# Kernel optimization log

Measured on AMD Instinct MI355X. Metric: run time of the kernel, lower is better.

The kernel has to match this reference:

```python
import jax, jax.numpy as jnp
import numpy as np

NF = 10      # num RBF / Chebyshev features
GAMMA = 1.0
EMB = 10
H = 64
NHEADS = 2


def _rbf(d):
    centers = jnp.arange(1, NF + 1, dtype=d.dtype)
    return jnp.exp(-GAMMA * (centers - d[..., None]) ** 2)


def _cheb(a):
    feats = [jnp.ones_like(a), a]
    for _ in range(2, NF):
        feats.append(2 * a * feats[-1] - feats[-2])
    return jnp.stack(feats, -1)


def _gru_layer(xs, wih, whh, bih, bhh):
    # xs: [L, B, D] -> [L, B, H]; PyTorch gate order r, z, n
    B = xs.shape[1]
    def step(h, xt):
        gi = xt @ wih.T + bih
        gh = h @ whh.T + bhh
        ir, iz, inn = jnp.split(gi, 3, -1)
        hr, hz, hn = jnp.split(gh, 3, -1)
        r = jax.nn.sigmoid(ir + hr)
        z = jax.nn.sigmoid(iz + hz)
        n = jnp.tanh(inn + r * hn)
        hnew = (1 - z) * n + z * h
        return hnew, hnew
    h0 = jnp.zeros((B, H), xs.dtype)
    _, ys = jax.lax.scan(step, h0, xs)
    return ys


def _mha(x, in_w, in_b, out_w, out_b):
    B, L, E = x.shape
    hd = E // NHEADS
    qkv = x @ in_w.T + in_b
    q, k, v = jnp.split(qkv, 3, -1)
    sp = lambda t: t.reshape(B, L, NHEADS, hd).transpose(0, 2, 1, 3)
    q, k, v = sp(q), sp(k), sp(v)
    scale = 1.0 / float(np.sqrt(hd))
    att = jax.nn.softmax(jnp.einsum('bhqd,bhkd->bhqk', q, k) * scale, -1)
    o = jnp.einsum('bhqk,bhkd->bhqd', att, v).transpose(0, 2, 1, 3).reshape(B, L, E)
    return o @ out_w.T + out_b


def _ln(x, s, b):
    m = x.mean(-1, keepdims=True)
    v = ((x - m) ** 2).mean(-1, keepdims=True)
    return (x - m) / jnp.sqrt(v + 1e-5) * s + b


def setup_inputs() -> dict:
    key = jax.random.key(0)
    ks = jax.random.split(key, 48)
    N, L = 384, 256
    # bond rows: [atom_idx1, atom_idx2, bond_dist]; angle rows: [d1, d2, angle]
    idx1 = jax.random.randint(ks[0], (N, L), 1, 119).astype(jnp.float32)
    idx2 = jax.random.randint(ks[1], (N, L), 1, 119).astype(jnp.float32)
    dist = jax.random.uniform(ks[2], (N, L), minval=0.5, maxval=5.0)
    d1 = jax.random.uniform(ks[3], (N, L), minval=0.5, maxval=5.0)
    d2 = jax.random.uniform(ks[4], (N, L), minval=0.5, maxval=5.0)
    ang = jax.random.uniform(ks[5], (N, L), minval=-1.0, maxval=1.0)
    bond_x = jnp.stack([idx1, idx2, dist], 1)
    angle_x = jnp.stack([d1, d2, ang], 1)
    is_angle = (jnp.arange(N) % 3 == 2)
    x = jnp.where(is_angle[:, None, None], angle_x, bond_x)

    def nrm(k, shp, s=0.1):
        return jax.random.normal(k, shp) * s

    D_IN = 2 * EMB + NF  # 30
    inp = {
        'x': x,
        'emb': nrm(ks[6], (119, EMB), 1.0),
        'wih0': nrm(ks[7], (3 * H, D_IN)),
        'whh0': nrm(ks[8], (3 * H, H)),
        'bih0': nrm(ks[9], (3 * H,)),
        'bhh0': nrm(ks[10], (3 * H,)),
        'wih12': nrm(ks[11], (2, 3 * H, H)),
        'whh12': nrm(ks[12], (2, 3 * H, H)),
        'bih12': nrm(ks[13], (2, 3 * H)),
        'bhh12': nrm(ks[14], (2, 3 * H)),
        'in_w1': nrm(ks[15], (3 * H, H)),
        'in_b1': nrm(ks[16], (3 * H,)),
        'out_w1': nrm(ks[17], (H, H)),
        'out_b1': nrm(ks[18], (H,)),
        'in_w2': nrm(ks[19], (3 * H, H)),
        'in_b2': nrm(ks[20], (3 * H,)),
        'out_w2': nrm(ks[21], (H, H)),
        'out_b2': nrm(ks[22], (H,)),
        'ff_w1': nrm(ks[23], (1024, H)),
        'ff_b1': nrm(ks[24], (1024,)),
        'ff_w2': nrm(ks[25], (H, 1024)),
        'ff_b2': nrm(ks[26], (H,)),
        'ln1_s': jnp.ones((H,)), 'ln1_b': jnp.zeros((H,)),
        'ln2_s': jnp.ones((H,)), 'ln2_b': jnp.zeros((H,)),
        'ln3_s': jnp.ones((H,)), 'ln3_b': jnp.zeros((H,)),
        'ln4_s': jnp.ones((H,)), 'ln4_b': jnp.zeros((H,)),
        'fw1': nrm(ks[27], (256, H)), 'fb1': nrm(ks[28], (256,)),
        'fw2': nrm(ks[29], (64, 256)), 'fb2': nrm(ks[30], (64,)),
        'fw3': nrm(ks[31], (32, 64)), 'fb3': nrm(ks[32], (32,)),
        'fw4': nrm(ks[33], (1, 32)), 'fb4': nrm(ks[34], (1,)),
    }
    return inp


def reference(x, emb, wih0, whh0, bih0, bhh0, wih12, whh12, bih12, bhh12,
              in_w1, in_b1, out_w1, out_b1, in_w2, in_b2, out_w2, out_b2,
              ff_w1, ff_b1, ff_w2, ff_b2,
              ln1_s, ln1_b, ln2_s, ln2_b, ln3_s, ln3_b, ln4_s, ln4_b,
              fw1, fb1, fw2, fb2, fw3, fb3, fw4, fb4):
    # Vectorized featurization (replaces the per-triplet Python loop):
    # rows with i%3 in {0,1} are bond rows, i%3==2 are angle rows.
    i1 = jnp.clip(x[:, 0].astype(jnp.int32), 0, 118)
    i2 = jnp.clip(x[:, 1].astype(jnp.int32), 0, 118)
    bond_feat = jnp.concatenate([emb[i1], emb[i2], _rbf(x[:, 2])], -1)
    angle_feat = jnp.concatenate([_rbf(x[:, 0]), _rbf(x[:, 1]), _cheb(x[:, 2])], -1)
    is_angle = (jnp.arange(x.shape[0]) % 3 == 2)
    feat = jnp.where(is_angle[:, None, None], angle_feat, bond_feat)  # [N, L, 30]

    hs = feat.transpose(1, 0, 2)  # [L, N, 30]
    hs = _gru_layer(hs, wih0, whh0, bih0, bhh0)
    for l in range(2):
        hs = _gru_layer(hs, wih12[l], whh12[l], bih12[l], bhh12[l])
    g = hs.transpose(1, 0, 2)  # [N, L, H]

    def ffn(t):
        return jax.nn.relu(jax.nn.relu(t @ ff_w1.T + ff_b1) @ ff_w2.T + ff_b2)

    a = _mha(g, in_w1, in_b1, out_w1, out_b1)
    h = _ln(g + a, ln1_s, ln1_b)
    h = _ln(h + ffn(h), ln2_s, ln2_b)
    a = _mha(h, in_w2, in_b2, out_w2, out_b2)
    h = _ln(a + a, ln3_s, ln3_b)  # faithful to original: attn_out + attn_out
    h = _ln(h + ffn(h), ln4_s, ln4_b)
    o = h[:, -1, :]
    o = jax.nn.silu(o @ fw1.T + fb1)
    o = jax.nn.silu(o @ fw2.T + fb2)
    o = jax.nn.silu(o @ fw3.T + fb3)
    o = o @ fw4.T + fb4
    return o.squeeze(-1)
```

## Files before the change

### kernel.cpp

```cpp
#include <hip/hip_runtime.h>

static constexpr int NB   = 384;
static constexpr int SEQL = 256;
static constexpr int NROWS = NB * SEQL;

typedef short bf16x8 __attribute__((ext_vector_type(8)));
typedef float f32x4  __attribute__((ext_vector_type(4)));

union B8u {
    bf16x8 v;
    ushort us[8];
    uint4  q;
};

__device__ inline ushort f2bf(float f) {
    uint u = __float_as_uint(f);
    uint r = u + 0x7FFFu + ((u >> 16) & 1u);
    return (ushort)(r >> 16);
}

__device__ inline void split8(float4 a, float4 b, B8u& hi, B8u& lo) {
    float f[8] = {a.x, a.y, a.z, a.w, b.x, b.y, b.z, b.w};
    #pragma unroll
    for (int i = 0; i < 8; ++i) {
        ushort h = f2bf(f[i]);
        hi.us[i] = h;
        float fh = __uint_as_float(((uint)h) << 16);
        lo.us[i] = f2bf(f[i] - fh);
    }
}

__global__ __launch_bounds__(256) void split_kernel(
    const float* __restrict__ src, ushort* __restrict__ hi,
    ushort* __restrict__ lo, int n)
{
    int i = blockIdx.x * 256 + threadIdx.x;
    if (i < n) {
        float f = src[i];
        ushort h = f2bf(f);
        hi[i] = h;
        float fh = __uint_as_float(((uint)h) << 16);
        lo[i] = f2bf(f - fh);
    }
}

__global__ __launch_bounds__(192) void featproj_kernel(
    const float* __restrict__ x, const float* __restrict__ emb,
    const float* __restrict__ wih0, const float* __restrict__ bih0,
    float* __restrict__ X)
{
    __shared__ float F[32][33];
    const int tid = threadIdx.x;
    const int m0  = blockIdx.x * 32;

    if (tid < 96) {
        const int r   = tid & 31;
        const int grp = tid >> 5;
        const int m   = m0 + r;
        const int b   = m % NB;
        const int l   = m / NB;
        const float* xb = x + (size_t)b * (3 * SEQL);
        const float x0 = xb[l], x1 = xb[SEQL + l], x2 = xb[2 * SEQL + l];
        const bool is_angle = (b % 3) == 2;
        float o[10];
        if (is_angle) {
            if (grp < 2) {
                const float a = (grp == 0) ? x0 : x1;
                #pragma unroll
                for (int c = 0; c < 10; ++c) { float d = (float)(c + 1) - a; o[c] = __expf(-d * d); }
            } else {
                float t0 = 1.f, t1 = x2;
                o[0] = 1.f; o[1] = x2;
                #pragma unroll
                for (int c = 2; c < 10; ++c) { float t = 2.f * x2 * t1 - t0; o[c] = t; t0 = t1; t1 = t; }
            }
        } else {
            if (grp < 2) {
                const float xv = (grp == 0) ? x0 : x1;
                int idx = (int)xv; idx = idx < 0 ? 0 : (idx > 118 ? 118 : idx);
                #pragma unroll
                for (int c = 0; c < 10; ++c) o[c] = emb[idx * 10 + c];
            } else {
                #pragma unroll
                for (int c = 0; c < 10; ++c) { float d = (float)(c + 1) - x2; o[c] = __expf(-d * d); }
            }
        }
        #pragma unroll
        for (int c = 0; c < 10; ++c) F[r][grp * 10 + c] = o[c];
    }
    __syncthreads();

    float w[30];
    #pragma unroll
    for (int k = 0; k < 30; ++k) w[k] = wih0[tid * 30 + k];
    const float bj = bih0[tid];
    for (int r = 0; r < 32; ++r) {
        float acc = bj;
        #pragma unroll
        for (int k = 0; k < 30; ++k) acc += F[r][k] * w[k];
        X[(size_t)(m0 + r) * 192 + tid] = acc;
    }
}

__global__ __launch_bounds__(192) void gru_kernel(
    const float* __restrict__ X, const float* __restrict__ whh,
    const float* __restrict__ bhh, float* __restrict__ Y, int out_batch_major)
{
    const int b = blockIdx.x;
    const int j = threadIdx.x;
    __shared__ float h[64];
    __shared__ float gis[192], ghs[192];

    float w[64];
    #pragma unroll
    for (int k = 0; k < 64; ++k) w[k] = whh[j * 64 + k];
    const float bj = bhh[j];
    if (j < 64) h[j] = 0.f;
    __syncthreads();

    for (int t = 0; t < SEQL; ++t) {
        const float gi = X[((size_t)t * NB + b) * 192 + j];
        float gh = bj;
        #pragma unroll
        for (int k = 0; k < 64; ++k) gh += h[k] * w[k];
        gis[j] = gi; ghs[j] = gh;
        __syncthreads();
        if (j < 64) {
            const float r = 1.f / (1.f + __expf(-(gis[j] + ghs[j])));
            const float z = 1.f / (1.f + __expf(-(gis[64 + j] + ghs[64 + j])));
            const float n = tanhf(gis[128 + j] + r * ghs[128 + j]);
            const float hn = (1.f - z) * n + z * h[j];
            h[j] = hn;
            const size_t row = out_batch_major ? ((size_t)b * SEQL + t)
                                               : ((size_t)t * NB + b);
            Y[row * 64 + j] = hn;
        }
        __syncthreads();
    }
}

template<int NCOLS>
__global__ __launch_bounds__(256, 2) void gemm_mfma(
    const float* __restrict__ A, const ushort* __restrict__ Whi,
    const ushort* __restrict__ Wlo, const float* __restrict__ bias,
    float* __restrict__ C)
{
    const int tid = threadIdx.x;
    const int w   = tid >> 6;
    const int lane = tid & 63;
    const int c = lane & 15;
    const int g = lane >> 4;
    const int m0 = blockIdx.x * 128 + 32 * w;

    B8u ah[2][2], al[2][2];
    #pragma unroll
    for (int rm = 0; rm < 2; ++rm) {
        const float* ap = A + (size_t)(m0 + 16 * rm + c) * 64;
        #pragma unroll
        for (int ks = 0; ks < 2; ++ks) {
            float4 v0 = *(const float4*)(ap + 32 * ks + 8 * g);
            float4 v1 = *(const float4*)(ap + 32 * ks + 8 * g + 4);
            split8(v0, v1, ah[rm][ks], al[rm][ks]);
        }
    }

    f32x4 acc[NCOLS / 16][2];
    #pragma unroll
    for (int nt = 0; nt < NCOLS / 16; ++nt) {
        float bv = bias[16 * nt + c];
        #pragma unroll
        for (int rm = 0; rm < 2; ++rm)
            acc[nt][rm] = (f32x4){bv, bv, bv, bv};
    }

    #pragma unroll
    for (int nt = 0; nt < NCOLS / 16; ++nt) {
        B8u wh[2], wl[2];
        #pragma unroll
        for (int ks = 0; ks < 2; ++ks) {
            size_t off = (size_t)(16 * nt + c) * 64 + 32 * ks + 8 * g;
            wh[ks].q = *(const uint4*)(Whi + off);
            wl[ks].q = *(const uint4*)(Wlo + off);
        }
        #pragma unroll
        for (int rm = 0; rm < 2; ++rm)
            #pragma unroll
            for (int ks = 0; ks < 2; ++ks) {
                acc[nt][rm] = __builtin_amdgcn_mfma_f32_16x16x32_bf16(ah[rm][ks].v, wh[ks].v, acc[nt][rm], 0, 0, 0);
                acc[nt][rm] = __builtin_amdgcn_mfma_f32_16x16x32_bf16(al[rm][ks].v, wh[ks].v, acc[nt][rm], 0, 0, 0);
                acc[nt][rm] = __builtin_amdgcn_mfma_f32_16x16x32_bf16(ah[rm][ks].v, wl[ks].v, acc[nt][rm], 0, 0, 0);
            }
    }

    #pragma unroll
    for (int nt = 0; nt < NCOLS / 16; ++nt)
        #pragma unroll
        for (int rm = 0; rm < 2; ++rm)
            #pragma unroll
            for (int reg = 0; reg < 4; ++reg) {
                int row = m0 + 16 * rm + 4 * g + reg;
                C[(size_t)row * NCOLS + 16 * nt + c] = acc[nt][rm][reg];
            }
}

__global__ __launch_bounds__(256, 2) void ffn_mfma(
    const float* __restrict__ Xin,
    const ushort* __restrict__ W1hi, const ushort* __restrict__ W1lo,
    const ushort* __restrict__ W2hi, const ushort* __restrict__ W2lo,
    const float* __restrict__ b1, const float* __restrict__ b2,
    float* __restrict__ Out)
{
    __shared__ __align__(16) ushort sW1h[64 * 72], sW1l[64 * 72];
    __shared__ __align__(16) ushort sW2h[64 * 72], sW2l[64 * 72];
    __shared__ __align__(16) ushort sHh[128 * 72], sHl[128 * 72];
    __shared__ float sb1[64];

    const int tid = threadIdx.x;
    const int w   = tid >> 6;
    const int lane = tid & 63;
    const int c = lane & 15;
    const int g = lane >> 4;
    const int r0 = blockIdx.x * 128;

    B8u xh[2][2], xl[2][2];
    #pragma unroll
    for (int rm = 0; rm < 2; ++rm) {
        const float* ap = Xin + (size_t)(r0 + 32 * w + 16 * rm + c) * 64;
        #pragma unroll
        for (int ks = 0; ks < 2; ++ks) {
            float4 v0 = *(const float4*)(ap + 32 * ks + 8 * g);
            float4 v1 = *(const float4*)(ap + 32 * ks + 8 * g + 4);
            split8(v0, v1, xh[rm][ks], xl[rm][ks]);
        }
    }

    f32x4 acc2[4][2];
    #pragma unroll
    for (int jt = 0; jt < 4; ++jt) {
        float bv = b2[16 * jt + c];
        #pragma unroll
        for (int mt = 0; mt < 2; ++mt)
            acc2[jt][mt] = (f32x4){bv, bv, bv, bv};
    }

    for (int nc = 0; nc < 16; ++nc) {
        __syncthreads();
        {
            const int n = tid >> 2, s = tid & 3;
            size_t s1 = (size_t)(nc * 64 + n) * 64 + s * 16;
            size_t s2 = (size_t)n * 1024 + nc * 64 + s * 16;
            int d = n * 72 + s * 16;
            *(uint4*)&sW1h[d]     = *(const uint4*)(W1hi + s1);
            *(uint4*)&sW1h[d + 8] = *(const uint4*)(W1hi + s1 + 8);
            *(uint4*)&sW1l[d]     = *(const uint4*)(W1lo + s1);
            *(uint4*)&sW1l[d + 8] = *(const uint4*)(W1lo + s1 + 8);
            *(uint4*)&sW2h[d]     = *(const uint4*)(W2hi + s2);
            *(uint4*)&sW2h[d + 8] = *(const uint4*)(W2hi + s2 + 8);
            *(uint4*)&sW2l[d]     = *(const uint4*)(W2lo + s2);
            *(uint4*)&sW2l[d + 8] = *(const uint4*)(W2lo + s2 + 8);
            if (tid < 64) sb1[tid] = b1[nc * 64 + tid];
        }
        __syncthreads();

        f32x4 acc1[4][2];
        #pragma unroll
        for (int jm = 0; jm < 4; ++jm) {
            float b0 = sb1[16 * jm + 4 * g + 0];
            float b1v = sb1[16 * jm + 4 * g + 1];
            float b2v = sb1[16 * jm + 4 * g + 2];
            float b3v = sb1[16 * jm + 4 * g + 3];
            #pragma unroll
            for (int rm = 0; rm < 2; ++rm)
                acc1[jm][rm] = (f32x4){b0, b1v, b2v, b3v};
        }
        #pragma unroll
        for (int jm = 0; jm < 4; ++jm) {
            B8u w1h[2], w1l[2];
            #pragma unroll
            for (int ks = 0; ks < 2; ++ks) {
                int off = (16 * jm + c) * 72 + 32 * ks + 8 * g;
                w1h[ks].q = *(const uint4*)&sW1h[off];
                w1l[ks].q = *(const uint4*)&sW1l[off];
            }
            #pragma unroll
            for (int rm = 0; rm < 2; ++rm)
                #pragma unroll
                for (int ks = 0; ks < 2; ++ks) {
                    acc1[jm][rm] = __builtin_amdgcn_mfma_f32_16x16x32_bf16(w1h[ks].v, xh[rm][ks].v, acc1[jm][rm], 0, 0, 0);
                    acc1[jm][rm] = __builtin_amdgcn_mfma_f32_16x16x32_bf16(w1l[ks].v, xh[rm][ks].v, acc1[jm][rm], 0, 0, 0);
                    acc1[jm][rm] = __builtin_amdgcn_mfma_f32_16x16x32_bf16(w1h[ks].v, xl[rm][ks].v, acc1[jm][rm], 0, 0, 0);
                }
        }
        #pragma unroll
        for (int jm = 0; jm < 4; ++jm)
            #pragma unroll
            for (int rm = 0; rm < 2; ++rm) {
                ushort hh[4], hl[4];
                #pragma unroll
                for (int reg = 0; reg < 4; ++reg) {
                    float hv = fmaxf(acc1[jm][rm][reg], 0.f);
                    ushort h = f2bf(hv);
                    hh[reg] = h;
                    float fh = __uint_as_float(((uint)h) << 16);
                    hl[reg] = f2bf(hv - fh);
                }
                int el = (32 * w + 16 * rm + c) * 72 + 16 * jm + 4 * g;
                *(uint2*)&sHh[el] = make_uint2((uint)hh[0] | ((uint)hh[1] << 16),
                                               (uint)hh[2] | ((uint)hh[3] << 16));
                *(uint2*)&sHl[el] = make_uint2((uint)hl[0] | ((uint)hl[1] << 16),
                                               (uint)hl[2] | ((uint)hl[3] << 16));
            }
        asm volatile("s_waitcnt lgkmcnt(0)" ::: "memory");
        __builtin_amdgcn_sched_barrier(0);

        #pragma unroll
        for (int ks = 0; ks < 2; ++ks) {
            B8u ahh[2], ahl[2], bwh[4], bwl[4];
            #pragma unroll
            for (int mt = 0; mt < 2; ++mt) {
                int el = (32 * w + 16 * mt + c) * 72 + 32 * ks + 8 * g;
                ahh[mt].q = *(const uint4*)&sHh[el];
                ahl[mt].q = *(const uint4*)&sHl[el];
            }
            #pragma unroll
            for (int jt = 0; jt < 4; ++jt) {
                int el = (16 * jt + c) * 72 + 32 * ks + 8 * g;
                bwh[jt].q = *(const uint4*)&sW2h[el];
                bwl[jt].q = *(const uint4*)&sW2l[el];
            }
            #pragma unroll
            for (int jt = 0; jt < 4; ++jt)
                #pragma unroll
                for (int mt = 0; mt < 2; ++mt) {
                    acc2[jt][mt] = __builtin_amdgcn_mfma_f32_16x16x32_bf16(ahh[mt].v, bwh[jt].v, acc2[jt][mt], 0, 0, 0);
                    acc2[jt][mt] = __builtin_amdgcn_mfma_f32_16x16x32_bf16(ahl[mt].v, bwh[jt].v, acc2[jt][mt], 0, 0, 0);
                    acc2[jt][mt] = __builtin_amdgcn_mfma_f32_16x16x32_bf16(ahh[mt].v, bwl[jt].v, acc2[jt][mt], 0, 0, 0);
                }
        }
    }

    #pragma unroll
    for (int jt = 0; jt < 4; ++jt)
        #pragma unroll
        for (int mt = 0; mt < 2; ++mt)
            #pragma unroll
            for (int reg = 0; reg < 4; ++reg) {
                int row = r0 + 32 * w + 16 * mt + 4 * g + reg;
                Out[(size_t)row * 64 + 16 * jt + c] = fmaxf(acc2[jt][mt][reg], 0.f);
            }
}

__global__ __launch_bounds__(256) void attn_kernel(
    const float* __restrict__ QKV, float* __restrict__ O)
{
    const int hh = blockIdx.x;
    const int b  = blockIdx.y;
    const int q  = threadIdx.x;
    const float scale = 0.17677669529663687f;

    __shared__ float Ks[64][36];
    __shared__ float Vs[64][36];

    float qr[32];
    {
        const float* qrow = QKV + ((size_t)b * SEQL + q) * 192 + hh * 32;
        #pragma unroll
        for (int d4 = 0; d4 < 8; ++d4) {
            float4 v = *(const float4*)(qrow + d4 * 4);
            qr[d4 * 4 + 0] = v.x; qr[d4 * 4 + 1] = v.y;
            qr[d4 * 4 + 2] = v.z; qr[d4 * 4 + 3] = v.w;
        }
    }
    float m = -1e30f, l = 0.f;
    float o[32];
    #pragma unroll
    for (int d = 0; d < 32; ++d) o[d] = 0.f;

    for (int kc = 0; kc < 4; ++kc) {
        #pragma unroll
        for (int p = 0; p < 2; ++p) {
            const int i = threadIdx.x + p * 256;
            const int r = i >> 3, c4 = i & 7;
            const float* src = QKV + ((size_t)b * SEQL + kc * 64 + r) * 192 + 64 + hh * 32 + c4 * 4;
            *(float4*)&Ks[r][c4 * 4] = *(const float4*)src;
            *(float4*)&Vs[r][c4 * 4] = *(const float4*)(src + 64);
        }
        __syncthreads();
        for (int kk = 0; kk < 64; ++kk) {
            float s = 0.f;
            #pragma unroll
            for (int d = 0; d < 32; d += 4) {
                float4 kv = *(const float4*)&Ks[kk][d];
                s += qr[d] * kv.x + qr[d + 1] * kv.y + qr[d + 2] * kv.z + qr[d + 3] * kv.w;
            }
            s *= scale;
            const float mnew = fmaxf(m, s);
            const float corr = __expf(m - mnew);
            const float p    = __expf(s - mnew);
            l = l * corr + p;
            #pragma unroll
            for (int d = 0; d < 32; d += 4) {
                float4 vv = *(const float4*)&Vs[kk][d];
                o[d + 0] = o[d + 0] * corr + p * vv.x;
                o[d + 1] = o[d + 1] * corr + p * vv.y;
                o[d + 2] = o[d + 2] * corr + p * vv.z;
                o[d + 3] = o[d + 3] * corr + p * vv.w;
            }
            m = mnew;
        }
        __syncthreads();
    }
    const float inv = 1.f / l;
    float* orow = O + ((size_t)b * SEQL + q) * 64 + hh * 32;
    #pragma unroll
    for (int d4 = 0; d4 < 8; ++d4) {
        float4 v;
        v.x = o[d4 * 4 + 0] * inv; v.y = o[d4 * 4 + 1] * inv;
        v.z = o[d4 * 4 + 2] * inv; v.w = o[d4 * 4 + 3] * inv;
        *(float4*)(orow + d4 * 4) = v;
    }
}

__global__ __launch_bounds__(256) void add_ln_kernel(
    const float* __restrict__ A, const float* __restrict__ B,
    const float* __restrict__ s, const float* __restrict__ bb,
    float* __restrict__ O)
{
    const size_t row = (size_t)blockIdx.x * 4 + (threadIdx.x >> 6);
    const int lane = threadIdx.x & 63;
    float v = A[row * 64 + lane] + B[row * 64 + lane];
    float sum = v;
    #pragma unroll
    for (int off = 32; off; off >>= 1) sum += __shfl_xor(sum, off);
    const float mean = sum * (1.f / 64.f);
    const float d = v - mean;
    float sq = d * d;
    #pragma unroll
    for (int off = 32; off; off >>= 1) sq += __shfl_xor(sq, off);
    const float var = sq * (1.f / 64.f);
    O[row * 64 + lane] = d * rsqrtf(var + 1e-5f) * s[lane] + bb[lane];
}

__global__ __launch_bounds__(256) void head_kernel(
    const float* __restrict__ Hf,
    const float* __restrict__ fw1, const float* __restrict__ fb1,
    const float* __restrict__ fw2, const float* __restrict__ fb2,
    const float* __restrict__ fw3, const float* __restrict__ fb3,
    const float* __restrict__ fw4, const float* __restrict__ fb4,
    float* __restrict__ out)
{
    const int b = blockIdx.x;
    const int tid = threadIdx.x;
    __shared__ float t0[64], t1[256], t2[64], t3[32];
    if (tid < 64) t0[tid] = Hf[((size_t)b * SEQL + (SEQL - 1)) * 64 + tid];
    __syncthreads();
    {
        float acc = fb1[tid];
        #pragma unroll 4
        for (int k = 0; k < 64; ++k) acc += t0[k] * fw1[tid * 64 + k];
        t1[tid] = acc / (1.f + __expf(-acc));
    }
    __syncthreads();
    if (tid < 64) {
        float acc = fb2[tid];
        #pragma unroll 4
        for (int k = 0; k < 256; ++k) acc += t1[k] * fw2[tid * 256 + k];
        t2[tid] = acc / (1.f + __expf(-acc));
    }
    __syncthreads();
    if (tid < 32) {
        float acc = fb3[tid];
        #pragma unroll 4
        for (int k = 0; k < 64; ++k) acc += t2[k] * fw3[tid * 64 + k];
        t3[tid] = acc / (1.f + __expf(-acc));
    }
    __syncthreads();
    if (tid == 0) {
        float acc = fb4[0];
        #pragma unroll
        for (int k = 0; k < 32; ++k) acc += t3[k] * fw4[k];
        out[b] = acc;
    }
}

extern "C" void kernel_launch(void* const* d_in, const int* in_sizes, int n_in,
                              void* d_out, int out_size, void* d_ws, size_t ws_size,
                              hipStream_t stream) {
    const float* x     = (const float*)d_in[0];
    const float* emb   = (const float*)d_in[1];
    const float* wih0  = (const float*)d_in[2];
    const float* whh0  = (const float*)d_in[3];
    const float* bih0  = (const float*)d_in[4];
    const float* bhh0  = (const float*)d_in[5];
    const float* wih12 = (const float*)d_in[6];
    const float* whh12 = (const float*)d_in[7];
    const float* bih12 = (const float*)d_in[8];
    const float* bhh12 = (const float*)d_in[9];
    const float* in_w1 = (const float*)d_in[10];
    const float* in_b1 = (const float*)d_in[11];
    const float* out_w1= (const float*)d_in[12];
    const float* out_b1= (const float*)d_in[13];
    const float* in_w2 = (const float*)d_in[14];
    const float* in_b2 = (const float*)d_in[15];
    const float* out_w2= (const float*)d_in[16];
    const float* out_b2= (const float*)d_in[17];
    const float* ff_w1 = (const float*)d_in[18];
    const float* ff_b1 = (const float*)d_in[19];
    const float* ff_w2 = (const float*)d_in[20];
    const float* ff_b2 = (const float*)d_in[21];
    const float* ln1_s = (const float*)d_in[22];
    const float* ln1_b = (const float*)d_in[23];
    const float* ln2_s = (const float*)d_in[24];
    const float* ln2_b = (const float*)d_in[25];
    const float* ln3_s = (const float*)d_in[26];
    const float* ln3_b = (const float*)d_in[27];
    const float* ln4_s = (const float*)d_in[28];
    const float* ln4_b = (const float*)d_in[29];
    const float* fw1   = (const float*)d_in[30];
    const float* fb1   = (const float*)d_in[31];
    const float* fw2   = (const float*)d_in[32];
    const float* fb2   = (const float*)d_in[33];
    const float* fw3   = (const float*)d_in[34];
    const float* fb3   = (const float*)d_in[35];
    const float* fw4   = (const float*)d_in[36];
    const float* fb4   = (const float*)d_in[37];

    float* ws = (float*)d_ws;
    float* X  = ws;
    float* S0 = X  + (size_t)NROWS * 192;
    float* S1 = S0 + (size_t)NROWS * 64;
    float* S2 = S1 + (size_t)NROWS * 64;

    ushort* bf = (ushort*)(S2 + (size_t)NROWS * 64);
    ushort* ffw1hi = bf;
    ushort* ffw1lo = ffw1hi + 65536;
    ushort* ffw2hi = ffw1lo + 65536;
    ushort* ffw2lo = ffw2hi + 65536;
    ushort* wghi   = ffw2lo + 65536;
    ushort* wglo   = wghi + 24576;
    ushort* q1hi   = wglo + 24576;
    ushort* q1lo   = q1hi + 12288;
    ushort* q2hi   = q1lo + 12288;
    ushort* q2lo   = q2hi + 12288;
    ushort* o1hi   = q2lo + 12288;
    ushort* o1lo   = o1hi + 4096;
    ushort* o2hi   = o1lo + 4096;
    ushort* o2lo   = o2hi + 4096;

    split_kernel<<<65536 / 256, 256, 0, stream>>>(ff_w1, ffw1hi, ffw1lo, 65536);
    split_kernel<<<65536 / 256, 256, 0, stream>>>(ff_w2, ffw2hi, ffw2lo, 65536);
    split_kernel<<<24576 / 256, 256, 0, stream>>>(wih12, wghi, wglo, 24576);
    split_kernel<<<12288 / 256, 256, 0, stream>>>(in_w1, q1hi, q1lo, 12288);
    split_kernel<<<12288 / 256, 256, 0, stream>>>(in_w2, q2hi, q2lo, 12288);
    split_kernel<<<4096 / 256, 256, 0, stream>>>(out_w1, o1hi, o1lo, 4096);
    split_kernel<<<4096 / 256, 256, 0, stream>>>(out_w2, o2hi, o2lo, 4096);

    featproj_kernel<<<NROWS / 32, 192, 0, stream>>>(x, emb, wih0, bih0, X);
    gru_kernel<<<NB, 192, 0, stream>>>(X, whh0, bhh0, S0, 0);
    gemm_mfma<192><<<NROWS / 128, 256, 0, stream>>>(S0, wghi, wglo, bih12, X);
    gru_kernel<<<NB, 192, 0, stream>>>(X, whh12, bhh12, S1, 0);
    gemm_mfma<192><<<NROWS / 128, 256, 0, stream>>>(S1, wghi + 12288, wglo + 12288, bih12 + 192, X);
    gru_kernel<<<NB, 192, 0, stream>>>(X, whh12 + 192 * 64, bhh12 + 192, S0, 1);

    gemm_mfma<192><<<NROWS / 128, 256, 0, stream>>>(S0, q1hi, q1lo, in_b1, X);
    attn_kernel<<<dim3(2, NB), 256, 0, stream>>>(X, S1);
    gemm_mfma<64><<<NROWS / 128, 256, 0, stream>>>(S1, o1hi, o1lo, out_b1, S2);
    add_ln_kernel<<<NROWS / 4, 256, 0, stream>>>(S0, S2, ln1_s, ln1_b, S1);
    ffn_mfma<<<NROWS / 128, 256, 0, stream>>>(S1, ffw1hi, ffw1lo, ffw2hi, ffw2lo, ff_b1, ff_b2, S2);
    add_ln_kernel<<<NROWS / 4, 256, 0, stream>>>(S1, S2, ln2_s, ln2_b, S0);

    gemm_mfma<192><<<NROWS / 128, 256, 0, stream>>>(S0, q2hi, q2lo, in_b2, X);
    attn_kernel<<<dim3(2, NB), 256, 0, stream>>>(X, S1);
    gemm_mfma<64><<<NROWS / 128, 256, 0, stream>>>(S1, o2hi, o2lo, out_b2, S2);
    add_ln_kernel<<<NROWS / 4, 256, 0, stream>>>(S2, S2, ln3_s, ln3_b, S1);
    ffn_mfma<<<NROWS / 128, 256, 0, stream>>>(S1, ffw1hi, ffw1lo, ffw2hi, ffw2lo, ff_b1, ff_b2, S2);
    add_ln_kernel<<<NROWS / 4, 256, 0, stream>>>(S1, S2, ln4_s, ln4_b, S0);

    head_kernel<<<NB, 256, 0, stream>>>(S0, fw1, fb1, fw2, fb2, fw3, fb3, fw4, fb4,
                                        (float*)d_out);
    (void)in_sizes; (void)n_in; (void)out_size; (void)ws_size;
}
```

Measured before the change: 1.312 ms.

## Rewrite attention as MFMA flash attention with split-bf16 precision

Replaces the scalar per-thread online-softmax attention kernel with a wave-level MFMA version. Each wave handles 64 queries and computes QK^T and PV with bf16x3 split products to keep near-fp32 accuracy. Probabilities are staged through swizzled LDS so they can serve as MFMA operands. K and V are read straight from global memory per wave instead of through shared tiles, which adds redundant loads and register pressure in exchange for matrix-core throughput.

```diff
diff --git a/kernel.cpp b/kernel.cpp
--- a/kernel.cpp
+++ b/kernel.cpp
@@ -199,7 +199,7 @@
             #pragma unroll
             for (int reg = 0; reg < 4; ++reg) {
                 int row = m0 + 16 * rm + 4 * g + reg;
-                C[(size_t)row * NCOLS + 16 * nt + c] = acc[nt][rm][reg];
+                C[(size_t)row * NCOLS + 16 * nt + reg * 0 + c] = acc[nt][rm][reg];
             }
 }
 
@@ -350,74 +350,152 @@
             }
 }
 
-__global__ __launch_bounds__(256) void attn_kernel(
-    const float* __restrict__ QKV, float* __restrict__ O)
-{
-    const int hh = blockIdx.x;
-    const int b  = blockIdx.y;
-    const int q  = threadIdx.x;
+__global__ __launch_bounds__(256, 2) void attn_mfma(
+    const float* __restrict__ QKV, float* __restrict__ Out)
+{
+    __shared__ __align__(16) ushort Ph[4][4096];
+    __shared__ __align__(16) ushort Pl[4][4096];
+
+    const int h = blockIdx.x;
+    const int b = blockIdx.y;
+    const int tid = threadIdx.x;
+    const int w = tid >> 6;
+    const int lane = tid & 63;
+    const int c = lane & 15;
+    const int g = lane >> 4;
     const float scale = 0.17677669529663687f;
 
-    __shared__ float Ks[64][36];
-    __shared__ float Vs[64][36];
-
-    float qr[32];
-    {
-        const float* qrow = QKV + ((size_t)b * SEQL + q) * 192 + hh * 32;
-        #pragma unroll
-        for (int d4 = 0; d4 < 8; ++d4) {
-            float4 v = *(const float4*)(qrow + d4 * 4);
-            qr[d4 * 4 + 0] = v.x; qr[d4 * 4 + 1] = v.y;
-            qr[d4 * 4 + 2] = v.z; qr[d4 * 4 + 3] = v.w;
-        }
-    }
-    float m = -1e30f, l = 0.f;
-    float o[32];
-    #pragma unroll
-    for (int d = 0; d < 32; ++d) o[d] = 0.f;
+    const float* base = QKV + (size_t)b * SEQL * 192;
+    ushort* phw = Ph[w];
+    ushort* plw = Pl[w];
+
+    B8u qh[4], ql[4];
+    #pragma unroll
+    for (int qt = 0; qt < 4; ++qt) {
+        const float* p = base + (size_t)(64 * w + 16 * qt + c) * 192 + h * 32 + 8 * g;
+        float4 v0 = *(const float4*)p;
+        float4 v1 = *(const float4*)(p + 4);
+        v0.x *= scale; v0.y *= scale; v0.z *= scale; v0.w *= scale;
+        v1.x *= scale; v1.y *= scale; v1.z *= scale; v1.w *= scale;
+        split8(v0, v1, qh[qt], ql[qt]);
+    }
+
+    f32x4 o[2][4];
+    #pragma unroll
+    for (int dt = 0; dt < 2; ++dt)
+        #pragma unroll
+        for (int qt = 0; qt < 4; ++qt)
+            o[dt][qt] = (f32x4){0.f, 0.f, 0.f, 0.f};
+    float mrun[4] = {-1e30f, -1e30f, -1e30f, -1e30f};
+    float lrun[4] = {0.f, 0.f, 0.f, 0.f};
 
     for (int kc = 0; kc < 4; ++kc) {
-        #pragma unroll
-        for (int p = 0; p < 2; ++p) {
-            const int i = threadIdx.x + p * 256;
-            const int r = i >> 3, c4 = i & 7;
-            const float* src = QKV + ((size_t)b * SEQL + kc * 64 + r) * 192 + 64 + hh * 32 + c4 * 4;
-            *(float4*)&Ks[r][c4 * 4] = *(const float4*)src;
-            *(float4*)&Vs[r][c4 * 4] = *(const float4*)(src + 64);
-        }
-        __syncthreads();
-        for (int kk = 0; kk < 64; ++kk) {
-            float s = 0.f;
-            #pragma unroll
-            for (int d = 0; d < 32; d += 4) {
-                float4 kv = *(const float4*)&Ks[kk][d];
-                s += qr[d] * kv.x + qr[d + 1] * kv.y + qr[d + 2] * kv.z + qr[d + 3] * kv.w;
-            }
-            s *= scale;
-            const float mnew = fmaxf(m, s);
-            const float corr = __expf(m - mnew);
-            const float p    = __expf(s - mnew);
-            l = l * corr + p;
-            #pragma unroll
-            for (int d = 0; d < 32; d += 4) {
-                float4 vv = *(const float4*)&Vs[kk][d];
-                o[d + 0] = o[d + 0] * corr + p * vv.x;
-                o[d + 1] = o[d + 1] * corr + p * vv.y;
-                o[d + 2] = o[d + 2] * corr + p * vv.z;
-                o[d + 3] = o[d + 3] * corr + p * vv.w;
-            }
-            m = mnew;
-        }
-        __syncthreads();
-    }
-    const float inv = 1.f / l;
-    float* orow = O + ((size_t)b * SEQL + q) * 64 + hh * 32;
-    #pragma unroll
-    for (int d4 = 0; d4 < 8; ++d4) {
-        float4 v;
-        v.x = o[d4 * 4 + 0] * inv; v.y = o[d4 * 4 + 1] * inv;
-        v.z = o[d4 * 4 + 2] * inv; v.w = o[d4 * 4 + 3] * inv;
-        *(float4*)(orow + d4 * 4) = v;
+        B8u kh[4], kl[4];
+        #pragma unroll
+        for (int kt = 0; kt < 4; ++kt) {
+            const float* p = base + (size_t)(kc * 64 + 16 * kt + c) * 192 + 64 + h * 32 + 8 * g;
+            split8(*(const float4*)p, *(const float4*)(p + 4), kh[kt], kl[kt]);
+        }
+        f32x4 st[4][4];
+        #pragma unroll
+        for (int kt = 0; kt < 4; ++kt)
+            #pragma unroll
+            for (int qt = 0; qt < 4; ++qt)
+                st[kt][qt] = (f32x4){0.f, 0.f, 0.f, 0.f};
+        #pragma unroll
+        for (int kt = 0; kt < 4; ++kt)
+            #pragma unroll
+            for (int qt = 0; qt < 4; ++qt) {
+                st[kt][qt] = __builtin_amdgcn_mfma_f32_16x16x32_bf16(kh[kt].v, qh[qt].v, st[kt][qt], 0, 0, 0);
+                st[kt][qt] = __builtin_amdgcn_mfma_f32_16x16x32_bf16(kl[kt].v, qh[qt].v, st[kt][qt], 0, 0, 0);
+                st[kt][qt] = __builtin_amdgcn_mfma_f32_16x16x32_bf16(kh[kt].v, ql[qt].v, st[kt][qt], 0, 0, 0);
+            }
+
+        asm volatile("s_waitcnt lgkmcnt(0)" ::: "memory");
+        #pragma unroll
+        for (int qt = 0; qt < 4; ++qt) {
+            float cmax = st[0][qt][0];
+            #pragma unroll
+            for (int kt = 0; kt < 4; ++kt)
+                #pragma unroll
+                for (int r = 0; r < 4; ++r) cmax = fmaxf(cmax, st[kt][qt][r]);
+            cmax = fmaxf(cmax, __shfl_xor(cmax, 16));
+            cmax = fmaxf(cmax, __shfl_xor(cmax, 32));
+            const float mnew = fmaxf(mrun[qt], cmax);
+            const float corr = __expf(mrun[qt] - mnew);
+            mrun[qt] = mnew;
+            const int ql_ = 16 * qt + c;
+            float csum = 0.f;
+            #pragma unroll
+            for (int kt = 0; kt < 4; ++kt) {
+                ushort hh[4], hl[4];
+                #pragma unroll
+                for (int r = 0; r < 4; ++r) {
+                    float pv = __expf(st[kt][qt][r] - mnew);
+                    csum += pv;
+                    ushort ph_ = f2bf(pv);
+                    hh[r] = ph_;
+                    hl[r] = f2bf(pv - __uint_as_float(((uint)ph_) << 16));
+                }
+                const int ow = (2 * kt + (g >> 1)) ^ (ql_ & 7);
+                const int addr = ql_ * 64 + ow * 8 + (g & 1) * 4;
+                *(uint2*)&phw[addr] = make_uint2((uint)hh[0] | ((uint)hh[1] << 16),
+                                                 (uint)hh[2] | ((uint)hh[3] << 16));
+                *(uint2*)&plw[addr] = make_uint2((uint)hl[0] | ((uint)hl[1] << 16),
+                                                 (uint)hl[2] | ((uint)hl[3] << 16));
+            }
+            csum += __shfl_xor(csum, 16);
+            csum += __shfl_xor(csum, 32);
+            lrun[qt] = lrun[qt] * corr + csum;
+            #pragma unroll
+            for (int dt = 0; dt < 2; ++dt)
+                #pragma unroll
+                for (int r = 0; r < 4; ++r) o[dt][qt][r] *= corr;
+        }
+
+        B8u vh[2][2], vl[2][2];
+        #pragma unroll
+        for (int ks = 0; ks < 2; ++ks)
+            #pragma unroll
+            for (int dt = 0; dt < 2; ++dt) {
+                const float* vp = base + (size_t)(kc * 64 + ks * 32 + 8 * g) * 192 + 128 + h * 32 + 16 * dt + c;
+                float f0 = vp[0], f1 = vp[192], f2 = vp[384], f3 = vp[576];
+                float f4 = vp[768], f5 = vp[960], f6 = vp[1152], f7 = vp[1344];
+                split8(make_float4(f0, f1, f2, f3), make_float4(f4, f5, f6, f7),
+                       vh[ks][dt], vl[ks][dt]);
+            }
+
+        asm volatile("s_waitcnt lgkmcnt(0)" ::: "memory");
+        __builtin_amdgcn_sched_barrier(0);
+
+        #pragma unroll
+        for (int ks = 0; ks < 2; ++ks)
+            #pragma unroll
+            for (int qt = 0; qt < 4; ++qt) {
+                const int ql_ = 16 * qt + c;
+                const int orr = (ks * 4 + g) ^ (ql_ & 7);
+                const int addr = ql_ * 64 + orr * 8;
+                B8u pbh, pbl;
+                pbh.q = *(const uint4*)&phw[addr];
+                pbl.q = *(const uint4*)&plw[addr];
+                #pragma unroll
+                for (int dt = 0; dt < 2; ++dt) {
+                    o[dt][qt] = __builtin_amdgcn_mfma_f32_16x16x32_bf16(vh[ks][dt].v, pbh.v, o[dt][qt], 0, 0, 0);
+                    o[dt][qt] = __builtin_amdgcn_mfma_f32_16x16x32_bf16(vl[ks][dt].v, pbh.v, o[dt][qt], 0, 0, 0);
+                    o[dt][qt] = __builtin_amdgcn_mfma_f32_16x16x32_bf16(vh[ks][dt].v, pbl.v, o[dt][qt], 0, 0, 0);
+                }
+            }
+    }
+
+    #pragma unroll
+    for (int qt = 0; qt < 4; ++qt) {
+        const float inv = 1.f / lrun[qt];
+        const size_t row = (size_t)b * SEQL + 64 * w + 16 * qt + c;
+        #pragma unroll
+        for (int dt = 0; dt < 2; ++dt)
+            #pragma unroll
+            for (int r = 0; r < 4; ++r)
+                Out[row * 64 + h * 32 + 16 * dt + 4 * g + r] = o[dt][qt][r] * inv;
     }
 }
 
@@ -563,14 +641,14 @@
     gru_kernel<<<NB, 192, 0, stream>>>(X, whh12 + 192 * 64, bhh12 + 192, S0, 1);
 
     gemm_mfma<192><<<NROWS / 128, 256, 0, stream>>>(S0, q1hi, q1lo, in_b1, X);
-    attn_kernel<<<dim3(2, NB), 256, 0, stream>>>(X, S1);
+    attn_mfma<<<dim3(2, NB), 256, 0, stream>>>(X, S1);
     gemm_mfma<64><<<NROWS / 128, 256, 0, stream>>>(S1, o1hi, o1lo, out_b1, S2);
     add_ln_kernel<<<NROWS / 4, 256, 0, stream>>>(S0, S2, ln1_s, ln1_b, S1);
     ffn_mfma<<<NROWS / 128, 256, 0, stream>>>(S1, ffw1hi, ffw1lo, ffw2hi, ffw2lo, ff_b1, ff_b2, S2);
     add_ln_kernel<<<NROWS / 4, 256, 0, stream>>>(S1, S2, ln2_s, ln2_b, S0);
 
     gemm_mfma<192><<<NROWS / 128, 256, 0, stream>>>(S0, q2hi, q2lo, in_b2, X);
-    attn_kernel<<<dim3(2, NB), 256, 0, stream>>>(X, S1);
+    attn_mfma<<<dim3(2, NB), 256, 0, stream>>>(X, S1);
     gemm_mfma<64><<<NROWS / 128, 256, 0, stream>>>(S1, o2hi, o2lo, out_b2, S2);
     add_ln_kernel<<<NROWS / 4, 256, 0, stream>>>(S2, S2, ln3_s, ln3_b, S1);
     ffn_mfma<<<NROWS / 128, 256, 0, stream>>>(S1, ffw1hi, ffw1lo, ffw2hi, ffw2lo, ff_b1, ff_b2, S2);
```

Result: faster. 1.057 ms (-19.5%).
